# Optimization experiments

Hardware: AMD Instinct MI355X
Metric: run time of the kernel (lower is better)

The kernel has to match this reference:

```python
import jax, jax.numpy as jnp
import numpy as np

B, S, H = 64, 2048, 512


def setup_inputs() -> dict:
    key = jax.random.key(0)
    k1, k2, k3, k4, k5 = jax.random.split(key, 5)
    scale = 1.0 / np.sqrt(H)
    return {
        "decoder_hidden": jax.random.normal(k1, (B, H), dtype=jnp.float32),
        "encoder_outputs": jax.random.normal(k2, (B, S, H), dtype=jnp.float32),
        "W_q": jax.random.normal(k3, (H, H), dtype=jnp.float32) * scale,
        "W_k": jax.random.normal(k4, (H, H), dtype=jnp.float32) * scale,
        "v": jax.random.normal(k5, (H,), dtype=jnp.float32) * scale,
    }


def reference(decoder_hidden, encoder_outputs, W_q, W_k, v):
    # query: [B,H] -> [B,1,H]; torch Linear computes x @ W.T
    query = (decoder_hidden @ W_q.T)[:, None, :]          # [B,1,H]
    keys = jnp.einsum('bsh,gh->bsg', encoder_outputs, W_k)  # [B,S,H]
    energy = jnp.tanh(query + keys)                        # [B,S,H]
    scores = jnp.einsum('bsh,h->bs', energy, v)            # [B,S]
    attention_weights = jax.nn.softmax(scores, axis=1)     # [B,S]
    context = jnp.einsum('bs,bsh->bh', attention_weights, encoder_outputs)
    return context, attention_weights
```

## Files before the change

### kernel.cpp

```cpp
#include <hip/hip_runtime.h>
#include <hip/hip_bf16.h>
#include <cstdint>


typedef __attribute__((ext_vector_type(8))) short short8;
typedef __attribute__((ext_vector_type(4))) float f32x4;

__device__ __forceinline__ unsigned short f2bf(float f) {
    unsigned u = __builtin_bit_cast(unsigned, f);
    u += 0x7FFFu + ((u >> 16) & 1u);
    return (unsigned short)(u >> 16);
}

__device__ __forceinline__ float tanh_fast(float x) {
    float e = __expf(2.0f * x);
    return 1.0f - 2.0f * __builtin_amdgcn_rcpf(e + 1.0f);
}

__device__ __forceinline__ void async16(const unsigned short* g, short* l) {
    __builtin_amdgcn_global_load_lds(
        (const __attribute__((address_space(1))) unsigned int*)g,
        (__attribute__((address_space(3))) unsigned int*)l, 16, 0, 0);
}

__global__ void cast_wk_kernel(const float* __restrict__ wk, unsigned short* __restrict__ wkb,
                               float* __restrict__ numer) {
    int i = (blockIdx.x * 256 + threadIdx.x) * 4;
    float4 f = *(const float4*)(wk + i);
    ushort4 o;
    o.x = f2bf(f.x); o.y = f2bf(f.y); o.z = f2bf(f.z); o.w = f2bf(f.w);
    *(ushort4*)(wkb + i) = o;
    if (blockIdx.x < 32) {
        *(float4*)(numer + i) = (float4){0.f, 0.f, 0.f, 0.f};
    }
}

__global__ void q_kernel(const float* __restrict__ dec, const float* __restrict__ wq,
                         float* __restrict__ q) {
    int b  = blockIdx.x >> 3;
    int g0 = (blockIdx.x & 7) * 64;
    int t = threadIdx.x, lane = t & 63, w = t >> 6;
    __shared__ float dls[512];
    dls[t] = dec[b * 512 + t];
    dls[t + 256] = dec[b * 512 + 256 + t];
    __syncthreads();
    #pragma unroll
    for (int gi = 0; gi < 16; ++gi) {
        int g = g0 + w + gi * 4;
        float acc = 0.f;
        #pragma unroll
        for (int it = 0; it < 2; ++it) {
            int h = (it * 64 + lane) * 4;
            float4 wv = *(const float4*)(wq + (size_t)g * 512 + h);
            acc += wv.x * dls[h] + wv.y * dls[h + 1] + wv.z * dls[h + 2] + wv.w * dls[h + 3];
        }
        #pragma unroll
        for (int m = 32; m; m >>= 1) acc += __shfl_xor(acc, m, 64);
        if (lane == 0) q[b * 512 + g] = acc;
    }
}

__launch_bounds__(256, 2)
__global__ void scores_kernel(const float* __restrict__ enc, const unsigned short* __restrict__ wkb,
                              const float* __restrict__ q, const float* __restrict__ v,
                              float* __restrict__ scores, float* __restrict__ numer) {
    __shared__ __align__(16) short Bs[512 * 32];
    __shared__ __align__(16) short As[64 * 40];
    __shared__ float q_s[512];
    __shared__ float v_s[512];
    __shared__ float red[4][64];
    __shared__ float w_lds[64];

    int t = threadIdx.x, lane = t & 63, w = t >> 6;
    int quad = lane >> 4, l15 = lane & 15;
    int tile = blockIdx.x;
    int b = tile >> 5;
    size_t m0 = (size_t)tile * 64;

    q_s[t] = q[b * 512 + t];   q_s[t + 256] = q[b * 512 + 256 + t];
    v_s[t] = v[t];             v_s[t + 256] = v[t + 256];

    f32x4 acc[4][8];
    #pragma unroll
    for (int i = 0; i < 4; ++i)
        #pragma unroll
        for (int j = 0; j < 8; ++j)
            acc[i][j] = (f32x4){0.f, 0.f, 0.f, 0.f};

    int arow = t >> 2, akq = t & 3;
    const float* aptr = enc + (m0 + arow) * 512 + akq * 8;

    int kqs = (lane & 3) ^ ((lane >> 3) & 3);
    const unsigned short* bgbase = wkb + (size_t)(w * 16 + (lane >> 2)) * 512 + kqs * 8;
    short* blbase = &Bs[(w * 16 + (lane >> 2)) * 32 + (lane & 3) * 8];

    for (int kk = 0; kk < 512; kk += 32) {
        __syncthreads();
        #pragma unroll
        for (int i = 0; i < 8; ++i)
            async16(bgbase + (size_t)i * 64 * 512 + kk, blbase + i * 64 * 32);
        float4 fa0 = *(const float4*)(aptr + kk);
        float4 fa1 = *(const float4*)(aptr + kk + 4);
        short8 av;
        av[0] = (short)f2bf(fa0.x); av[1] = (short)f2bf(fa0.y);
        av[2] = (short)f2bf(fa0.z); av[3] = (short)f2bf(fa0.w);
        av[4] = (short)f2bf(fa1.x); av[5] = (short)f2bf(fa1.y);
        av[6] = (short)f2bf(fa1.z); av[7] = (short)f2bf(fa1.w);
        *(short8*)&As[arow * 40 + akq * 8] = av;
        __syncthreads();

        short8 af[4];
        #pragma unroll
        for (int mt = 0; mt < 4; ++mt)
            af[mt] = *(short8*)&As[(mt * 16 + l15) * 40 + quad * 8];
        #pragma unroll
        for (int nt = 0; nt < 8; ++nt) {
            int brow = w * 128 + nt * 16 + l15;
            short8 bf = *(short8*)&Bs[brow * 32 + (quad ^ ((l15 >> 1) & 3)) * 8];
            #pragma unroll
            for (int mt = 0; mt < 4; ++mt)
                acc[mt][nt] = __builtin_amdgcn_mfma_f32_16x16x32_bf16(af[mt], bf, acc[mt][nt], 0, 0, 0);
        }
    }

    float rs[4][4];
    #pragma unroll
    for (int mt = 0; mt < 4; ++mt)
        #pragma unroll
        for (int r = 0; r < 4; ++r) rs[mt][r] = 0.f;
    #pragma unroll
    for (int nt = 0; nt < 8; ++nt) {
        int g = w * 128 + nt * 16 + l15;
        float qb = q_s[g], vv = v_s[g];
        #pragma unroll
        for (int mt = 0; mt < 4; ++mt)
            #pragma unroll
            for (int r = 0; r < 4; ++r)
                rs[mt][r] += tanh_fast(qb + acc[mt][nt][r]) * vv;
    }
    #pragma unroll
    for (int m = 1; m <= 8; m <<= 1)
        #pragma unroll
        for (int mt = 0; mt < 4; ++mt)
            #pragma unroll
            for (int r = 0; r < 4; ++r)
                rs[mt][r] += __shfl_xor(rs[mt][r], m, 64);
    if (l15 == 0) {
        #pragma unroll
        for (int mt = 0; mt < 4; ++mt)
            #pragma unroll
            for (int r = 0; r < 4; ++r)
                red[w][mt * 16 + quad * 4 + r] = rs[mt][r];
    }
    __syncthreads();
    if (t < 64) {
        float sc = red[0][t] + red[1][t] + red[2][t] + red[3][t];
        scores[m0 + t] = sc;
        w_lds[t] = __expf(sc);
    }
    __syncthreads();

    {
        float n0 = 0.f, n1 = 0.f;
        const float* ep = enc + m0 * 512 + t * 2;
        #pragma unroll 16
        for (int s = 0; s < 64; ++s) {
            float wv = w_lds[s];
            float2 e = *(const float2*)(ep + (size_t)s * 512);
            n0 += wv * e.x; n1 += wv * e.y;
        }
        float* np = numer + b * 512 + t * 2;
        atomicAdd(np, n0);
        atomicAdd(np + 1, n1);
    }
}

__global__ void softmax_kernel(float* __restrict__ out, const float* __restrict__ numer) {
    int b = blockIdx.x, t = threadIdx.x, lane = t & 63, w = t >> 6;
    float* sc = out + 32768 + b * 2048;
    __shared__ float wred[4];
    float vals[8];
    float mx = -1e30f;
    #pragma unroll
    for (int i = 0; i < 8; ++i) { vals[i] = sc[t + i * 256]; mx = fmaxf(mx, vals[i]); }
    #pragma unroll
    for (int m = 32; m; m >>= 1) mx = fmaxf(mx, __shfl_xor(mx, m, 64));
    if (lane == 0) wred[w] = mx;
    __syncthreads();
    mx = fmaxf(fmaxf(wred[0], wred[1]), fmaxf(wred[2], wred[3]));
    __syncthreads();
    float s = 0.f;
    #pragma unroll
    for (int i = 0; i < 8; ++i) { vals[i] = __expf(vals[i] - mx); s += vals[i]; }
    #pragma unroll
    for (int m = 32; m; m >>= 1) s += __shfl_xor(s, m, 64);
    if (lane == 0) wred[w] = s;
    __syncthreads();
    s = wred[0] + wred[1] + wred[2] + wred[3];
    float inv = 1.0f / s;
    #pragma unroll
    for (int i = 0; i < 8; ++i) sc[t + i * 256] = vals[i] * inv;
    float csc = __expf(-mx) * inv;
    out[b * 512 + t]       = numer[b * 512 + t] * csc;
    out[b * 512 + 256 + t] = numer[b * 512 + 256 + t] * csc;
}

extern "C" void kernel_launch(void* const* d_in, const int* in_sizes, int n_in,
                              void* d_out, int out_size, void* d_ws, size_t ws_size,
                              hipStream_t stream) {
    const float* dec = (const float*)d_in[0];
    const float* enc = (const float*)d_in[1];
    const float* wq  = (const float*)d_in[2];
    const float* wk  = (const float*)d_in[3];
    const float* v   = (const float*)d_in[4];
    float* out = (float*)d_out;

    unsigned short* wkb = (unsigned short*)d_ws;
    float* q = (float*)((char*)d_ws + 512 * 512 * 2);
    float* numer = (float*)((char*)d_ws + 512 * 512 * 2 + 64 * 512 * 4);

    cast_wk_kernel<<<256, 256, 0, stream>>>(wk, wkb, numer);
    q_kernel<<<512, 256, 0, stream>>>(dec, wq, q);
    scores_kernel<<<2048, 256, 0, stream>>>(enc, wkb, q, v, out + 32768, numer);
    softmax_kernel<<<64, 256, 0, stream>>>(out, numer);
}
```

Baseline: 452.5 us.

## Double-buffer LDS tiles in scores GEMM to overlap loads with MFMA

Turns the A and B shared-memory tiles into two buffers each. The next K-slice's global loads (async W_k copy to LDS and fp32 encoder reads) are issued before the MFMAs on the current slice. One barrier per iteration replaces two. This hides global load latency behind compute, at the cost of roughly double the LDS use, which may limit occupancy.

```diff
diff --git a/kernel.cpp b/kernel.cpp
--- a/kernel.cpp
+++ b/kernel.cpp
@@ -64,8 +64,8 @@
 __global__ void scores_kernel(const float* __restrict__ enc, const unsigned short* __restrict__ wkb,
                               const float* __restrict__ q, const float* __restrict__ v,
                               float* __restrict__ scores, float* __restrict__ numer) {
-    __shared__ __align__(16) short Bs[512 * 32];
-    __shared__ __align__(16) short As[64 * 40];
+    __shared__ __align__(16) short Bs[2][512 * 32];
+    __shared__ __align__(16) short As[2][64 * 40];
     __shared__ float q_s[512];
     __shared__ float v_s[512];
     __shared__ float red[4][64];
@@ -92,35 +92,58 @@
 
     int kqs = (lane & 3) ^ ((lane >> 3) & 3);
     const unsigned short* bgbase = wkb + (size_t)(w * 16 + (lane >> 2)) * 512 + kqs * 8;
-    short* blbase = &Bs[(w * 16 + (lane >> 2)) * 32 + (lane & 3) * 8];
-
-    for (int kk = 0; kk < 512; kk += 32) {
-        __syncthreads();
-        #pragma unroll
-        for (int i = 0; i < 8; ++i)
-            async16(bgbase + (size_t)i * 64 * 512 + kk, blbase + i * 64 * 32);
-        float4 fa0 = *(const float4*)(aptr + kk);
-        float4 fa1 = *(const float4*)(aptr + kk + 4);
+    int blo = (w * 16 + (lane >> 2)) * 32 + (lane & 3) * 8;
+    short* blbase0 = &Bs[0][blo];
+    short* blbase1 = &Bs[1][blo];
+
+    float4 nfa0 = *(const float4*)(aptr);
+    float4 nfa1 = *(const float4*)(aptr + 4);
+    #pragma unroll
+    for (int i = 0; i < 8; ++i)
+        async16(bgbase + (size_t)i * 64 * 512, blbase0 + i * 64 * 32);
+    {
         short8 av;
-        av[0] = (short)f2bf(fa0.x); av[1] = (short)f2bf(fa0.y);
-        av[2] = (short)f2bf(fa0.z); av[3] = (short)f2bf(fa0.w);
-        av[4] = (short)f2bf(fa1.x); av[5] = (short)f2bf(fa1.y);
-        av[6] = (short)f2bf(fa1.z); av[7] = (short)f2bf(fa1.w);
-        *(short8*)&As[arow * 40 + akq * 8] = av;
-        __syncthreads();
-
+        av[0] = (short)f2bf(nfa0.x); av[1] = (short)f2bf(nfa0.y);
+        av[2] = (short)f2bf(nfa0.z); av[3] = (short)f2bf(nfa0.w);
+        av[4] = (short)f2bf(nfa1.x); av[5] = (short)f2bf(nfa1.y);
+        av[6] = (short)f2bf(nfa1.z); av[7] = (short)f2bf(nfa1.w);
+        *(short8*)&As[0][arow * 40 + akq * 8] = av;
+    }
+    __syncthreads();
+
+    #pragma unroll
+    for (int ks = 0; ks < 16; ++ks) {
+        const int cur = ks & 1, nxt = cur ^ 1;
+        const int kk = ks * 32;
+        if (ks < 15) {
+            nfa0 = *(const float4*)(aptr + kk + 32);
+            nfa1 = *(const float4*)(aptr + kk + 36);
+            short* bl = nxt ? blbase1 : blbase0;
+            #pragma unroll
+            for (int i = 0; i < 8; ++i)
+                async16(bgbase + (size_t)i * 64 * 512 + kk + 32, bl + i * 64 * 32);
+        }
         short8 af[4];
         #pragma unroll
         for (int mt = 0; mt < 4; ++mt)
-            af[mt] = *(short8*)&As[(mt * 16 + l15) * 40 + quad * 8];
+            af[mt] = *(short8*)&As[cur][(mt * 16 + l15) * 40 + quad * 8];
         #pragma unroll
         for (int nt = 0; nt < 8; ++nt) {
             int brow = w * 128 + nt * 16 + l15;
-            short8 bf = *(short8*)&Bs[brow * 32 + (quad ^ ((l15 >> 1) & 3)) * 8];
+            short8 bf = *(short8*)&Bs[cur][brow * 32 + (quad ^ ((l15 >> 1) & 3)) * 8];
             #pragma unroll
             for (int mt = 0; mt < 4; ++mt)
                 acc[mt][nt] = __builtin_amdgcn_mfma_f32_16x16x32_bf16(af[mt], bf, acc[mt][nt], 0, 0, 0);
         }
+        if (ks < 15) {
+            short8 av;
+            av[0] = (short)f2bf(nfa0.x); av[1] = (short)f2bf(nfa0.y);
+            av[2] = (short)f2bf(nfa0.z); av[3] = (short)f2bf(nfa0.w);
+            av[4] = (short)f2bf(nfa1.x); av[5] = (short)f2bf(nfa1.y);
+            av[6] = (short)f2bf(nfa1.z); av[7] = (short)f2bf(nfa1.w);
+            *(short8*)&As[nxt][arow * 40 + akq * 8] = av;
+        }
+        __syncthreads();
     }
 
     float rs[4][4];
```

New measurement: 447.3 us. No clear change (-1.1%).

## Load W_k fragments directly to registers and stage encoder tile in two halves

Applied to the files above, without the earlier changes.

Replaces the per-k-step LDS staging of the bf16 W_k tile with direct global-to-register loads of MFMA B fragments, double-buffered across k-steps. The encoder A tile is converted to bf16 and written to LDS in two halves of 256 columns, which cuts the synchronisations from two per k-step to a few in total. This trades LDS traffic and barriers for more VGPR pressure (two register buffers of eight B fragments) and uncoalesced-per-lane 16-byte global loads of W_k that rely on L2/L1 reuse across blocks. A larger LDS footprint for A (8x64x40 shorts) replaces the old B buffer.

```diff
diff --git a/kernel.cpp b/kernel.cpp
--- a/kernel.cpp
+++ b/kernel.cpp
@@ -12,15 +12,18 @@
     return (unsigned short)(u >> 16);
 }
 
+__device__ __forceinline__ short8 cvt8(float4 a, float4 b) {
+    short8 r;
+    r[0] = (short)f2bf(a.x); r[1] = (short)f2bf(a.y);
+    r[2] = (short)f2bf(a.z); r[3] = (short)f2bf(a.w);
+    r[4] = (short)f2bf(b.x); r[5] = (short)f2bf(b.y);
+    r[6] = (short)f2bf(b.z); r[7] = (short)f2bf(b.w);
+    return r;
+}
+
 __device__ __forceinline__ float tanh_fast(float x) {
     float e = __expf(2.0f * x);
     return 1.0f - 2.0f * __builtin_amdgcn_rcpf(e + 1.0f);
-}
-
-__device__ __forceinline__ void async16(const unsigned short* g, short* l) {
-    __builtin_amdgcn_global_load_lds(
-        (const __attribute__((address_space(1))) unsigned int*)g,
-        (__attribute__((address_space(3))) unsigned int*)l, 16, 0, 0);
 }
 
 __global__ void cast_wk_kernel(const float* __restrict__ wk, unsigned short* __restrict__ wkb,
@@ -64,8 +67,7 @@
 __global__ void scores_kernel(const float* __restrict__ enc, const unsigned short* __restrict__ wkb,
                               const float* __restrict__ q, const float* __restrict__ v,
                               float* __restrict__ scores, float* __restrict__ numer) {
-    __shared__ __align__(16) short Bs[512 * 32];
-    __shared__ __align__(16) short As[64 * 40];
+    __shared__ __align__(16) short As[8][64][40];
     __shared__ float q_s[512];
     __shared__ float v_s[512];
     __shared__ float red[4][64];
@@ -89,38 +91,53 @@
 
     int arow = t >> 2, akq = t & 3;
     const float* aptr = enc + (m0 + arow) * 512 + akq * 8;
-
-    int kqs = (lane & 3) ^ ((lane >> 3) & 3);
-    const unsigned short* bgbase = wkb + (size_t)(w * 16 + (lane >> 2)) * 512 + kqs * 8;
-    short* blbase = &Bs[(w * 16 + (lane >> 2)) * 32 + (lane & 3) * 8];
-
-    for (int kk = 0; kk < 512; kk += 32) {
-        __syncthreads();
-        #pragma unroll
-        for (int i = 0; i < 8; ++i)
-            async16(bgbase + (size_t)i * 64 * 512 + kk, blbase + i * 64 * 32);
-        float4 fa0 = *(const float4*)(aptr + kk);
-        float4 fa1 = *(const float4*)(aptr + kk + 4);
-        short8 av;
-        av[0] = (short)f2bf(fa0.x); av[1] = (short)f2bf(fa0.y);
-        av[2] = (short)f2bf(fa0.z); av[3] = (short)f2bf(fa0.w);
-        av[4] = (short)f2bf(fa1.x); av[5] = (short)f2bf(fa1.y);
-        av[6] = (short)f2bf(fa1.z); av[7] = (short)f2bf(fa1.w);
-        *(short8*)&As[arow * 40 + akq * 8] = av;
-        __syncthreads();
-
+    #pragma unroll
+    for (int h = 0; h < 8; ++h) {
+        float4 fa0 = *(const float4*)(aptr + h * 32);
+        float4 fa1 = *(const float4*)(aptr + h * 32 + 4);
+        *(short8*)&As[h][arow][akq * 8] = cvt8(fa0, fa1);
+    }
+
+    const unsigned short* bp[8];
+    #pragma unroll
+    for (int nt = 0; nt < 8; ++nt)
+        bp[nt] = wkb + (size_t)(w * 128 + nt * 16 + l15) * 512 + quad * 8;
+
+    __syncthreads();
+
+    short8 bf[2][8];
+    #pragma unroll
+    for (int nt = 0; nt < 8; ++nt)
+        bf[0][nt] = *(const short8*)(bp[nt]);
+
+    #pragma unroll
+    for (int ks = 0; ks < 16; ++ks) {
+        const int cur = ks & 1, nxt = cur ^ 1;
+        const int kk = ks * 32;
+        if (ks == 8) {
+            __syncthreads();
+            #pragma unroll
+            for (int h = 0; h < 8; ++h) {
+                float4 fa0 = *(const float4*)(aptr + 256 + h * 32);
+                float4 fa1 = *(const float4*)(aptr + 256 + h * 32 + 4);
+                *(short8*)&As[h][arow][akq * 8] = cvt8(fa0, fa1);
+            }
+            __syncthreads();
+        }
+        if (ks < 15) {
+            #pragma unroll
+            for (int nt = 0; nt < 8; ++nt)
+                bf[nxt][nt] = *(const short8*)(bp[nt] + kk + 32);
+        }
         short8 af[4];
         #pragma unroll
         for (int mt = 0; mt < 4; ++mt)
-            af[mt] = *(short8*)&As[(mt * 16 + l15) * 40 + quad * 8];
-        #pragma unroll
-        for (int nt = 0; nt < 8; ++nt) {
-            int brow = w * 128 + nt * 16 + l15;
-            short8 bf = *(short8*)&Bs[brow * 32 + (quad ^ ((l15 >> 1) & 3)) * 8];
+            af[mt] = *(short8*)&As[ks & 7][mt * 16 + l15][quad * 8];
+        #pragma unroll
+        for (int nt = 0; nt < 8; ++nt)
             #pragma unroll
             for (int mt = 0; mt < 4; ++mt)
-                acc[mt][nt] = __builtin_amdgcn_mfma_f32_16x16x32_bf16(af[mt], bf, acc[mt][nt], 0, 0, 0);
-        }
+                acc[mt][nt] = __builtin_amdgcn_mfma_f32_16x16x32_bf16(af[mt], bf[cur][nt], acc[mt][nt], 0, 0, 0);
     }
 
     float rs[4][4];
```

After: 507.2 us. 12.1% more time.
